# Kernel tuning notes

Measured on AMD Instinct MI355X. Metric: run time of the kernel, lower is better.

## Reference

```python
import jax, jax.numpy as jnp
import numpy as np

# Sizes
NC, NT, NP = 100000, 300000, 50000   # customers, transactions, products
F, DIMC = 8, 16                      # columns per table, per-column embed dim
D = F * DIMC                         # 128 = proj_dim (lazy SAGEConv in-channels)
L, R = 2, 4                          # gnn layers, relation types
OUT = 10                             # out_channels
EM, EI = 300000, 600000              # edges: customer-makes-transaction, product-in-transaction


def setup_inputs() -> dict:
    key = jax.random.key(0)
    ks = jax.random.split(key, 14)
    s = 0.05
    return {
        "x_c": jax.random.normal(ks[0], (NC, F), jnp.float32),
        "x_t": jax.random.normal(ks[1], (NT, F), jnp.float32),
        "x_p": jax.random.normal(ks[2], (NP, F), jnp.float32),
        # per-table per-column numeric embedders: scalar -> DIMC (w*x + b)
        "W_col": jax.random.normal(ks[3], (3, F, DIMC), jnp.float32) * s,
        "b_col": jax.random.normal(ks[4], (3, F, DIMC), jnp.float32) * s,
        # SAGEConv weights per layer per relation: lin_l (neighbor) and lin_r (root)
        "Wn": jax.random.normal(ks[5], (L, R, D, D), jnp.float32) * s,
        "Wr": jax.random.normal(ks[6], (L, R, D, D), jnp.float32) * s,
        "b_lin": jax.random.normal(ks[7], (L, R, D), jnp.float32) * s,
        "W_out": jax.random.normal(ks[8], (D, OUT), jnp.float32) * s,
        "b_out": jax.random.normal(ks[9], (OUT,), jnp.float32) * s,
        "e_makes_src": jax.random.randint(ks[10], (EM,), 0, NC, jnp.int32),
        "e_makes_dst": jax.random.randint(ks[11], (EM,), 0, NT, jnp.int32),
        "e_in_src": jax.random.randint(ks[12], (EI,), 0, NP, jnp.int32),
        "e_in_dst": jax.random.randint(ks[13], (EI,), 0, NT, jnp.int32),
    }


def _embed(x, W, b):
    # x: [N, F]; W,b: [F, DIMC] -> [N, F*DIMC] (concat of per-column embeddings)
    n = x.shape[0]
    return (x[:, :, None] * W[None] + b[None]).reshape(n, -1)


def _sage(x_src, x_dst, src, dst, Wn, Wr, b, n_dst):
    # SAGEConv(mean): out = mean_neigh(x_src) @ Wn + b + x_dst @ Wr
    msg = jax.ops.segment_sum(x_src[src], dst, num_segments=n_dst)
    cnt = jax.ops.segment_sum(jnp.ones(src.shape[0], x_src.dtype), dst, num_segments=n_dst)
    mean = msg / jnp.maximum(cnt, 1.0)[:, None]  # isolated nodes -> 0 message
    return mean @ Wn + x_dst @ Wr + b


def reference(x_c, x_t, x_p, W_col, b_col, Wn, Wr, b_lin, W_out, b_out,
              e_makes_src, e_makes_dst, e_in_src, e_in_dst):
    h_c = _embed(x_c, W_col[0], b_col[0])
    h_t = _embed(x_t, W_col[1], b_col[1])
    h_p = _embed(x_p, W_col[2], b_col[2])
    for l in range(L):
        # R0: customer -makes-> transaction
        o_t0 = _sage(h_c, h_t, e_makes_src, e_makes_dst, Wn[l, 0], Wr[l, 0], b_lin[l, 0], NT)
        # R1: transaction -rev_makes-> customer
        o_c = _sage(h_t, h_c, e_makes_dst, e_makes_src, Wn[l, 1], Wr[l, 1], b_lin[l, 1], NC)
        # R2: product -in-> transaction
        o_t2 = _sage(h_p, h_t, e_in_src, e_in_dst, Wn[l, 2], Wr[l, 2], b_lin[l, 2], NT)
        # R3: transaction -rev_in-> product
        o_p = _sage(h_t, h_p, e_in_dst, e_in_src, Wn[l, 3], Wr[l, 3], b_lin[l, 3], NP)
        # HeteroConv(aggr='mean'): mean over relations targeting each dst type
        h_c, h_t, h_p = o_c, 0.5 * (o_t0 + o_t2), o_p
    logits = h_t @ W_out + b_out  # target_table = 'transaction'
    return jax.nn.softmax(logits, axis=1)
```

## Files before the change

kernel.cpp:

```cpp
#include <hip/hip_runtime.h>

#define NCV 100000
#define NTV 300000
#define NPV 50000
#define DD 128
#define OUTC 10
#define EMV 300000
#define EIV 600000
#define YST 16
#define NHEADS (NCV + NPV + 2 * NTV)
#define HIB ((NHEADS + 255) / 256)
#define PTB ((3 * 1280 * 64) / 256)
#define NEB ((EIV + 255) / 256)
#define QB  ((7 * 1280 * 64) / 256)
#define GYB ((NCV + NPV + 255) / 256)

__device__ __forceinline__ float i2f(int v) { return __int_as_float(v); }

__global__ __launch_bounds__(256) void init_prepT(
    int* __restrict__ heads,
    const float* __restrict__ Wn10, const float* __restrict__ Wn12,
    const float* __restrict__ Wr10, const float* __restrict__ Wr12,
    const float* __restrict__ Wout, float* __restrict__ T) {
  int b = blockIdx.x;
  int tid = threadIdx.x;
  if (b < HIB) {
    int i = b * 256 + tid;
    if (i < NHEADS) heads[i] = -1;
    return;
  }
  int gw = ((b - HIB) * 256 + tid) >> 6;
  int lane = tid & 63;
  if (gw >= 3 * 1280) return;
  int mat = gw / 1280, r = gw % 1280, n = r / 10, o = r % 10;
  float s = 0.f;
  #pragma unroll
  for (int mi = 0; mi < 2; ++mi) {
    int m = lane + mi * 64;
    float w;
    if (mat == 0) w = Wn10[n * 128 + m];
    else if (mat == 1) w = Wn12[n * 128 + m];
    else w = 0.5f * (Wr10[n * 128 + m] + Wr12[n * 128 + m]);
    s += w * Wout[m * 10 + o];
  }
  #pragma unroll
  for (int d = 32; d; d >>= 1) s += __shfl_xor(s, d);
  if (lane == 0) T[gw] = s;
}

__global__ __launch_bounds__(256) void build_prepQ(
    const int* __restrict__ ems, const int* __restrict__ emd,
    const int* __restrict__ eis, const int* __restrict__ eid,
    const float* __restrict__ xt,
    int* __restrict__ head_c, int* __restrict__ head_p,
    int* __restrict__ heads_t,
    int4* __restrict__ cnm, int4* __restrict__ cni,
    int2* __restrict__ tn_m, int2* __restrict__ tn_i,
    const float* __restrict__ Wn01, const float* __restrict__ Wr01,
    const float* __restrict__ Wn03, const float* __restrict__ Wr03,
    const float* __restrict__ Wn00, const float* __restrict__ Wn02,
    const float* __restrict__ Wr00, const float* __restrict__ Wr02,
    const float* __restrict__ T, float* __restrict__ Q) {
  int b = blockIdx.x;
  int tid = threadIdx.x;
  if (b < NEB) {
    int e = b * 256 + tid;
    if (e < EMV) {
      int c = ems[e], t = emd[e];
      int cn = atomicExch(&head_c[c], e);
      int tn = atomicExch(&heads_t[2 * t], e);
      const int4* xr = (const int4*)(xt + (size_t)t * 8);
      int4 x0 = xr[0], x1 = xr[1];
      size_t bb = 4 * (size_t)e;
      cnm[bb]     = make_int4(cn, x0.x, x0.y, x0.z);
      cnm[bb + 1] = make_int4(x0.w, x1.x, x1.y, x1.z);
      cnm[bb + 2] = make_int4(x1.w, 0, 0, 0);
      tn_m[e] = make_int2(tn, c);
    }
    if (e < EIV) {
      int p = eis[e], t = eid[e];
      int pn = atomicExch(&head_p[p], e);
      int tn = atomicExch(&heads_t[2 * t + 1], e);
      const int4* xr = (const int4*)(xt + (size_t)t * 8);
      int4 x0 = xr[0], x1 = xr[1];
      size_t bb = 4 * (size_t)e;
      cni[bb]     = make_int4(pn, x0.x, x0.y, x0.z);
      cni[bb + 1] = make_int4(x0.w, x1.x, x1.y, x1.z);
      cni[bb + 2] = make_int4(x1.w, 0, 0, 0);
      tn_i[e] = make_int2(tn, p);
    }
    return;
  }

  int gw = ((b - NEB) * 256 + tid) >> 6;
  int lane = tid & 63;
  if (gw >= 7 * 1280) return;
  int q = gw / 1280, r = gw % 1280, k = r / 10, o = r % 10;
  const float* T1 = T, *T2 = T + 1280, *T3 = T + 2560;
  float s = 0.f;
  #pragma unroll
  for (int ni = 0; ni < 2; ++ni) {
    int n = lane + ni * 64;
    float w, t;
    switch (q) {
      case 0: w = Wn01[k * 128 + n]; t = T1[n * 10 + o]; break;
      case 1: w = Wr01[k * 128 + n]; t = T1[n * 10 + o]; break;
      case 2: w = Wn03[k * 128 + n]; t = T2[n * 10 + o]; break;
      case 3: w = Wr03[k * 128 + n]; t = T2[n * 10 + o]; break;
      case 4: w = Wn00[k * 128 + n]; t = T3[n * 10 + o]; break;
      case 5: w = Wn02[k * 128 + n]; t = T3[n * 10 + o]; break;
      default: w = Wr00[k * 128 + n] + Wr02[k * 128 + n]; t = T3[n * 10 + o]; break;
    }
    s += w * t;
  }
  #pragma unroll
  for (int d = 32; d; d >>= 1) s += __shfl_xor(s, d);
  if (lane == 0) Q[gw] = s;
}

__global__ __launch_bounds__(256) void prep_B_w(
    const float* __restrict__ Wcol, const float* __restrict__ bcol,
    const float* __restrict__ b_lin, const float* __restrict__ Wout,
    const float* __restrict__ bout, const float* __restrict__ T,
    const float* __restrict__ Q, float* __restrict__ B) {
  int gw = (blockIdx.x * 256 + threadIdx.x) >> 6;
  int lane = threadIdx.x & 63;
  if (gw >= 450) return;
  int r = gw / 10, o = gw % 10;
  const float* WcC = Wcol, *WcT = Wcol + 128, *WcP = Wcol + 256;
  const float* bC = bcol, *bT = bcol + 128, *bP = bcol + 256;
  const float* Q1 = Q, *Q2 = Q + 1280, *Q3 = Q + 2560, *Q4 = Q + 3840;
  const float* Q5 = Q + 5120, *Q6 = Q + 6400, *Q7 = Q + 7680;
  const float* T1 = T, *T2 = T + 1280, *T3 = T + 2560;
  const float* b00 = b_lin, *b01 = b_lin + 128, *b02 = b_lin + 256, *b03 = b_lin + 384;
  const float* b10 = b_lin + 512, *b12 = b_lin + 768;
  float s = 0.f;
  if (r < 8) {
    if (lane < 16) s = WcT[r * 16 + lane] * Q1[(r * 16 + lane) * 10 + o];
  } else if (r < 16) {
    int j = r - 8;
    if (lane < 16)
      s = WcC[j * 16 + lane] * (Q2[(j * 16 + lane) * 10 + o] + Q5[(j * 16 + lane) * 10 + o]);
  } else if (r == 16) {
    for (int k2 = lane; k2 < 128; k2 += 64) s += bT[k2] * Q1[k2 * 10 + o];
  } else if (r < 25) {
    int j = r - 17;
    if (lane < 16) s = WcT[j * 16 + lane] * Q3[(j * 16 + lane) * 10 + o];
  } else if (r < 33) {
    int j = r - 25;
    if (lane < 16)
      s = WcP[j * 16 + lane] * (Q4[(j * 16 + lane) * 10 + o] + Q6[(j * 16 + lane) * 10 + o]);
  } else if (r == 33) {
    for (int k2 = lane; k2 < 128; k2 += 64) s += bT[k2] * Q3[k2 * 10 + o];
  } else if (r < 42) {
    int j = r - 34;
    if (lane < 16) s = WcT[j * 16 + lane] * Q7[(j * 16 + lane) * 10 + o];
  } else if (r == 42) {
    for (int k2 = lane; k2 < 128; k2 += 64)
      s += bC[k2] * (Q2[k2 * 10 + o] + Q5[k2 * 10 + o]) + b01[k2] * T1[k2 * 10 + o];
  } else if (r == 43) {
    for (int k2 = lane; k2 < 128; k2 += 64)
      s += bP[k2] * (Q4[k2 * 10 + o] + Q6[k2 * 10 + o]) + b03[k2] * T2[k2 * 10 + o];
  } else {
    for (int n = lane; n < 128; n += 64)
      s += (b10[n] + b12[n]) * Wout[n * 10 + o] + bT[n] * Q7[n * 10 + o] +
           (b00[n] + b02[n]) * T3[n * 10 + o];
  }
  #pragma unroll
  for (int d = 32; d; d >>= 1) s += __shfl_xor(s, d);
  if (lane == 0) {
    float v = s * 0.5f;
    if (r == 44) v += bout[o];
    B[gw] = v;
  }
}

__global__ __launch_bounds__(256) void gather_y(
    const int* __restrict__ head_c, const int* __restrict__ head_p,
    const int4* __restrict__ cnm, const int4* __restrict__ cni,
    const float* __restrict__ xc, const float* __restrict__ xp,
    const float* __restrict__ B,
    float* __restrict__ y_c, float* __restrict__ y_p) {
  __shared__ float sB[340];
  int tid = threadIdx.x;
  for (int i = tid; i < 340; i += 256) sB[i] = B[i];
  __syncthreads();
  int i = blockIdx.x * 256 + tid;
  if (i >= NCV + NPV) return;
  bool isC = i < NCV;
  int idx = isC ? i : i - NCV;
  const int4* cn = isC ? cnm : cni;
  int e = isC ? head_c[idx] : head_p[idx];

  float acc[8] = {0.f, 0.f, 0.f, 0.f, 0.f, 0.f, 0.f, 0.f};
  float cnt = 0.f;
  while (e >= 0) {
    size_t bb = 4 * (size_t)e;
    int4 w0 = cn[bb];
    int4 w1 = cn[bb + 1];
    int4 w2 = cn[bb + 2];
    acc[0] += i2f(w0.y); acc[1] += i2f(w0.z); acc[2] += i2f(w0.w);
    acc[3] += i2f(w1.x); acc[4] += i2f(w1.y); acc[5] += i2f(w1.z); acc[6] += i2f(w1.w);
    acc[7] += i2f(w2.x);
    cnt += 1.f;
    e = w0.x;
  }

  const float* xo = (isC ? xc : xp) + (size_t)idx * 8;
  const float* Bs = sB + (isC ? 0 : 170);
  float gg = cnt > 0.f ? 1.f : 0.f;
  float inv = gg / fmaxf(cnt, 1.f);
  float lg[OUTC];
  #pragma unroll
  for (int o = 0; o < OUTC; ++o) lg[o] = gg * Bs[16 * 10 + o];
  #pragma unroll
  for (int r = 0; r < 8; ++r) {
    float zb = acc[r] * inv;
    float zo = xo[r];
    #pragma unroll
    for (int o = 0; o < OUTC; ++o)
      lg[o] += zb * Bs[r * 10 + o] + zo * Bs[(8 + r) * 10 + o];
  }
  float4* yv = (float4*)((isC ? y_c : y_p) + (size_t)idx * YST);
  yv[0] = make_float4(lg[0], lg[1], lg[2], lg[3]);
  yv[1] = make_float4(lg[4], lg[5], lg[6], lg[7]);
  yv[2] = make_float4(lg[8], lg[9], 0.f, 0.f);
  yv[3] = make_float4(0.f, 0.f, 0.f, 0.f);
}

__global__ __launch_bounds__(256) void gather_t(
    const float* __restrict__ y_c, const float* __restrict__ y_p,
    const float* __restrict__ xt,
    const int* __restrict__ heads_t,
    const int2* __restrict__ tn_m, const int2* __restrict__ tn_i,
    const float* __restrict__ B, float* __restrict__ out) {
  __shared__ float sB[110];
  int tid = threadIdx.x;
  for (int i = tid; i < 110; i += 256) sB[i] = B[340 + i];
  __syncthreads();
  int t = blockIdx.x * 256 + tid;
  if (t >= NTV) return;

  int2 ht = ((const int2*)heads_t)[t];
  int e1 = ht.x, e2 = ht.y;

  float sc[OUTC] = {0.f, 0.f, 0.f, 0.f, 0.f, 0.f, 0.f, 0.f, 0.f, 0.f};
  float sp[OUTC] = {0.f, 0.f, 0.f, 0.f, 0.f, 0.f, 0.f, 0.f, 0.f, 0.f};
  float dc = 0.f, dp = 0.f;
  while (e1 >= 0 || e2 >= 0) {
    if (e1 >= 0) {
      int2 v = tn_m[e1];
      const float* yr = y_c + (size_t)v.y * YST;
      float4 u = *(const float4*)yr;
      float4 w = *(const float4*)(yr + 4);
      float2 z = *(const float2*)(yr + 8);
      sc[0] += u.x; sc[1] += u.y; sc[2] += u.z; sc[3] += u.w;
      sc[4] += w.x; sc[5] += w.y; sc[6] += w.z; sc[7] += w.w;
      sc[8] += z.x; sc[9] += z.y;
      dc += 1.f;
      e1 = v.x;
    }
    if (e2 >= 0) {
      int2 v = tn_i[e2];
      const float* yr = y_p + (size_t)v.y * YST;
      float4 u = *(const float4*)yr;
      float4 w = *(const float4*)(yr + 4);
      float2 z = *(const float2*)(yr + 8);
      sp[0] += u.x; sp[1] += u.y; sp[2] += u.z; sp[3] += u.w;
      sp[4] += w.x; sp[5] += w.y; sp[6] += w.z; sp[7] += w.w;
      sp[8] += z.x; sp[9] += z.y;
      dp += 1.f;
      e2 = v.x;
    }
  }

  float Gc = dc > 0.f ? 1.f : 0.f, Gp = dp > 0.f ? 1.f : 0.f;
  float ivc = 1.f / fmaxf(dc, 1.f), ivp = 1.f / fmaxf(dp, 1.f);

  const float4* xp4 = (const float4*)(xt + (size_t)t * 8);
  float4 xa = xp4[0], xb = xp4[1];
  float xv[8] = {xa.x, xa.y, xa.z, xa.w, xb.x, xb.y, xb.z, xb.w};

  float lg[OUTC];
  #pragma unroll
  for (int o = 0; o < OUTC; ++o)
    lg[o] = sc[o] * ivc + sp[o] * ivp +
            Gc * sB[80 + o] + Gp * sB[90 + o] + sB[100 + o];
  #pragma unroll
  for (int r = 0; r < 8; ++r) {
    float xr = xv[r];
    #pragma unroll
    for (int o = 0; o < OUTC; ++o) lg[o] += xr * sB[r * 10 + o];
  }

  float m = lg[0];
  #pragma unroll
  for (int o = 1; o < OUTC; ++o) m = fmaxf(m, lg[o]);
  float s = 0.f;
  #pragma unroll
  for (int o = 0; o < OUTC; ++o) { lg[o] = __expf(lg[o] - m); s += lg[o]; }
  float invs = 1.0f / s;
  float* op = &out[(size_t)t * OUTC];
  #pragma unroll
  for (int o = 0; o < 5; ++o) {
    float2 p2; p2.x = lg[2 * o] * invs; p2.y = lg[2 * o + 1] * invs;
    *(float2*)&op[2 * o] = p2;
  }
}

extern "C" void kernel_launch(void* const* d_in, const int* in_sizes, int n_in,
                              void* d_out, int out_size, void* d_ws, size_t ws_size,
                              hipStream_t stream) {
  const float* x_c   = (const float*)d_in[0];
  const float* x_t   = (const float*)d_in[1];
  const float* x_p   = (const float*)d_in[2];
  const float* W_col = (const float*)d_in[3];
  const float* b_col = (const float*)d_in[4];
  const float* Wn    = (const float*)d_in[5];
  const float* Wr    = (const float*)d_in[6];
  const float* b_lin = (const float*)d_in[7];
  const float* W_out = (const float*)d_in[8];
  const float* b_out = (const float*)d_in[9];
  const int* e_m_src = (const int*)d_in[10];
  const int* e_m_dst = (const int*)d_in[11];
  const int* e_i_src = (const int*)d_in[12];
  const int* e_i_dst = (const int*)d_in[13];
  float* out = (float*)d_out;

  size_t cursor = 0;
  char* base = (char*)d_ws;
  auto alloc = [&](size_t bytes) {
    void* p = base + cursor;
    cursor += (bytes + 255) & ~(size_t)255;
    return p;
  };
  int* heads   = (int*)alloc((size_t)NHEADS * 4);
  int* head_c  = heads;
  int* head_p  = heads + NCV;
  int* heads_t = heads + NCV + NPV;
  int4* cnm = (int4*)alloc((size_t)EMV * 64);
  int4* cni = (int4*)alloc((size_t)EIV * 64);
  int2* tn_m = (int2*)alloc((size_t)EMV * 8);
  int2* tn_i = (int2*)alloc((size_t)EIV * 8);
  float* y_c = (float*)alloc((size_t)NCV * YST * 4);
  float* y_p = (float*)alloc((size_t)NPV * YST * 4);
  float* T   = (float*)alloc(3 * 1280 * 4);
  float* Q   = (float*)alloc(7 * 1280 * 4);
  float* B   = (float*)alloc(450 * 4);

  const float* Wn_l[2][4]; const float* Wr_l[2][4];
  for (int l = 0; l < 2; ++l)
    for (int r = 0; r < 4; ++r) {
      Wn_l[l][r] = Wn + (size_t)(l * 4 + r) * DD * DD;
      Wr_l[l][r] = Wr + (size_t)(l * 4 + r) * DD * DD;
    }

  init_prepT<<<HIB + PTB, 256, 0, stream>>>(
      heads, Wn_l[1][0], Wn_l[1][2], Wr_l[1][0], Wr_l[1][2], W_out, T);

  build_prepQ<<<NEB + QB, 256, 0, stream>>>(
      e_m_src, e_m_dst, e_i_src, e_i_dst, x_t,
      head_c, head_p, heads_t, cnm, cni, tn_m, tn_i,
      Wn_l[0][1], Wr_l[0][1], Wn_l[0][3], Wr_l[0][3],
      Wn_l[0][0], Wn_l[0][2], Wr_l[0][0], Wr_l[0][2], T, Q);

  prep_B_w<<<(450 * 64 + 255) / 256, 256, 0, stream>>>(
      W_col, b_col, b_lin, W_out, b_out, T, Q, B);

  gather_y<<<GYB, 256, 0, stream>>>(
      head_c, head_p, cnm, cni, x_c, x_p, B, y_c, y_p);

  gather_t<<<(NTV + 255) / 256, 256, 0, stream>>>(
      y_c, y_p, x_t, heads_t, tn_m, tn_i, B, out);
}
```

Measured before the change: 224.8 us.

## Fold Q precompute into B computation, removing the separate prep_B_w launch

Drops the intermediate Q matrices (weights multiplied into T) and instead has each B warp contract the column embedder coefficients with the layer-0 SAGE weights directly, then dot with T. This lets the B computation run inside the edge-building kernel, which removes one kernel launch and the Q buffer round trip. In exchange each B warp runs longer serial loops (up to 128 iterations over two weight matrices), which lengthens the tail of the fused kernel.

Result: no change. 224.0 us (-0.4%).

```diff
diff --git a/kernel.cpp b/kernel.cpp
--- a/kernel.cpp
+++ b/kernel.cpp
@@ -12,7 +12,7 @@
 #define HIB ((NHEADS + 255) / 256)
 #define PTB ((3 * 1280 * 64) / 256)
 #define NEB ((EIV + 255) / 256)
-#define QB  ((7 * 1280 * 64) / 256)
+#define BDB ((450 * 64 + 255) / 256)
 #define GYB ((NCV + NPV + 255) / 256)
 
 __device__ __forceinline__ float i2f(int v) { return __int_as_float(v); }
@@ -48,7 +48,7 @@
   if (lane == 0) T[gw] = s;
 }
 
-__global__ __launch_bounds__(256) void build_prepQ(
+__global__ __launch_bounds__(256) void build_prepB(
     const int* __restrict__ ems, const int* __restrict__ emd,
     const int* __restrict__ eis, const int* __restrict__ eid,
     const float* __restrict__ xt,
@@ -56,11 +56,11 @@
     int* __restrict__ heads_t,
     int4* __restrict__ cnm, int4* __restrict__ cni,
     int2* __restrict__ tn_m, int2* __restrict__ tn_i,
-    const float* __restrict__ Wn01, const float* __restrict__ Wr01,
-    const float* __restrict__ Wn03, const float* __restrict__ Wr03,
-    const float* __restrict__ Wn00, const float* __restrict__ Wn02,
-    const float* __restrict__ Wr00, const float* __restrict__ Wr02,
-    const float* __restrict__ T, float* __restrict__ Q) {
+    const float* __restrict__ Wn, const float* __restrict__ Wr,
+    const float* __restrict__ Wcol, const float* __restrict__ bcol,
+    const float* __restrict__ b_lin, const float* __restrict__ Wout,
+    const float* __restrict__ bout,
+    const float* __restrict__ T, float* __restrict__ B) {
   int b = blockIdx.x;
   int tid = threadIdx.x;
   if (b < NEB) {
@@ -94,82 +94,99 @@
 
   int gw = ((b - NEB) * 256 + tid) >> 6;
   int lane = tid & 63;
-  if (gw >= 7 * 1280) return;
-  int q = gw / 1280, r = gw % 1280, k = r / 10, o = r % 10;
-  const float* T1 = T, *T2 = T + 1280, *T3 = T + 2560;
-  float s = 0.f;
-  #pragma unroll
-  for (int ni = 0; ni < 2; ++ni) {
-    int n = lane + ni * 64;
-    float w, t;
-    switch (q) {
-      case 0: w = Wn01[k * 128 + n]; t = T1[n * 10 + o]; break;
-      case 1: w = Wr01[k * 128 + n]; t = T1[n * 10 + o]; break;
-      case 2: w = Wn03[k * 128 + n]; t = T2[n * 10 + o]; break;
-      case 3: w = Wr03[k * 128 + n]; t = T2[n * 10 + o]; break;
-      case 4: w = Wn00[k * 128 + n]; t = T3[n * 10 + o]; break;
-      case 5: w = Wn02[k * 128 + n]; t = T3[n * 10 + o]; break;
-      default: w = Wr00[k * 128 + n] + Wr02[k * 128 + n]; t = T3[n * 10 + o]; break;
-    }
-    s += w * t;
-  }
-  #pragma unroll
-  for (int d = 32; d; d >>= 1) s += __shfl_xor(s, d);
-  if (lane == 0) Q[gw] = s;
-}
-
-__global__ __launch_bounds__(256) void prep_B_w(
-    const float* __restrict__ Wcol, const float* __restrict__ bcol,
-    const float* __restrict__ b_lin, const float* __restrict__ Wout,
-    const float* __restrict__ bout, const float* __restrict__ T,
-    const float* __restrict__ Q, float* __restrict__ B) {
-  int gw = (blockIdx.x * 256 + threadIdx.x) >> 6;
-  int lane = threadIdx.x & 63;
   if (gw >= 450) return;
   int r = gw / 10, o = gw % 10;
+  int n0 = lane, n1 = lane + 64;
+
+  const float* Wn00 = Wn;               const float* Wn01 = Wn + 16384;
+  const float* Wn02 = Wn + 2 * 16384;   const float* Wn03 = Wn + 3 * 16384;
+  const float* Wr00 = Wr;               const float* Wr01 = Wr + 16384;
+  const float* Wr02 = Wr + 2 * 16384;   const float* Wr03 = Wr + 3 * 16384;
   const float* WcC = Wcol, *WcT = Wcol + 128, *WcP = Wcol + 256;
   const float* bC = bcol, *bT = bcol + 128, *bP = bcol + 256;
-  const float* Q1 = Q, *Q2 = Q + 1280, *Q3 = Q + 2560, *Q4 = Q + 3840;
-  const float* Q5 = Q + 5120, *Q6 = Q + 6400, *Q7 = Q + 7680;
-  const float* T1 = T, *T2 = T + 1280, *T3 = T + 2560;
   const float* b00 = b_lin, *b01 = b_lin + 128, *b02 = b_lin + 256, *b03 = b_lin + 384;
   const float* b10 = b_lin + 512, *b12 = b_lin + 768;
-  float s = 0.f;
+  const float* T1 = T, *T2 = T + 1280, *T3 = T + 2560;
+
+  float a1_0 = 0.f, a1_1 = 0.f;
+  float a2_0 = 0.f, a2_1 = 0.f;
+  float a3_0 = 0.f, a3_1 = 0.f;
+  float extra = 0.f;
+
   if (r < 8) {
-    if (lane < 16) s = WcT[r * 16 + lane] * Q1[(r * 16 + lane) * 10 + o];
+    for (int j = 0; j < 16; ++j) {
+      float c = WcT[r * 16 + j]; int k = r * 16 + j;
+      a1_0 += c * Wn01[k * 128 + n0]; a1_1 += c * Wn01[k * 128 + n1];
+    }
   } else if (r < 16) {
-    int j = r - 8;
-    if (lane < 16)
-      s = WcC[j * 16 + lane] * (Q2[(j * 16 + lane) * 10 + o] + Q5[(j * 16 + lane) * 10 + o]);
+    int j0 = r - 8;
+    for (int j = 0; j < 16; ++j) {
+      float c = WcC[j0 * 16 + j]; int k = j0 * 16 + j;
+      a1_0 += c * Wr01[k * 128 + n0]; a1_1 += c * Wr01[k * 128 + n1];
+      a3_0 += c * Wn00[k * 128 + n0]; a3_1 += c * Wn00[k * 128 + n1];
+    }
   } else if (r == 16) {
-    for (int k2 = lane; k2 < 128; k2 += 64) s += bT[k2] * Q1[k2 * 10 + o];
+    for (int k = 0; k < 128; ++k) {
+      float c = bT[k];
+      a1_0 += c * Wn01[k * 128 + n0]; a1_1 += c * Wn01[k * 128 + n1];
+    }
   } else if (r < 25) {
-    int j = r - 17;
-    if (lane < 16) s = WcT[j * 16 + lane] * Q3[(j * 16 + lane) * 10 + o];
+    int j0 = r - 17;
+    for (int j = 0; j < 16; ++j) {
+      float c = WcT[j0 * 16 + j]; int k = j0 * 16 + j;
+      a2_0 += c * Wn03[k * 128 + n0]; a2_1 += c * Wn03[k * 128 + n1];
+    }
   } else if (r < 33) {
-    int j = r - 25;
-    if (lane < 16)
-      s = WcP[j * 16 + lane] * (Q4[(j * 16 + lane) * 10 + o] + Q6[(j * 16 + lane) * 10 + o]);
+    int j0 = r - 25;
+    for (int j = 0; j < 16; ++j) {
+      float c = WcP[j0 * 16 + j]; int k = j0 * 16 + j;
+      a2_0 += c * Wr03[k * 128 + n0]; a2_1 += c * Wr03[k * 128 + n1];
+      a3_0 += c * Wn02[k * 128 + n0]; a3_1 += c * Wn02[k * 128 + n1];
+    }
   } else if (r == 33) {
-    for (int k2 = lane; k2 < 128; k2 += 64) s += bT[k2] * Q3[k2 * 10 + o];
+    for (int k = 0; k < 128; ++k) {
+      float c = bT[k];
+      a2_0 += c * Wn03[k * 128 + n0]; a2_1 += c * Wn03[k * 128 + n1];
+    }
   } else if (r < 42) {
-    int j = r - 34;
-    if (lane < 16) s = WcT[j * 16 + lane] * Q7[(j * 16 + lane) * 10 + o];
+    int j0 = r - 34;
+    for (int j = 0; j < 16; ++j) {
+      float c = WcT[j0 * 16 + j]; int k = j0 * 16 + j;
+      a3_0 += c * (Wr00[k * 128 + n0] + Wr02[k * 128 + n0]);
+      a3_1 += c * (Wr00[k * 128 + n1] + Wr02[k * 128 + n1]);
+    }
   } else if (r == 42) {
-    for (int k2 = lane; k2 < 128; k2 += 64)
-      s += bC[k2] * (Q2[k2 * 10 + o] + Q5[k2 * 10 + o]) + b01[k2] * T1[k2 * 10 + o];
+    for (int k = 0; k < 128; ++k) {
+      float c = bC[k];
+      a1_0 += c * Wr01[k * 128 + n0]; a1_1 += c * Wr01[k * 128 + n1];
+      a3_0 += c * Wn00[k * 128 + n0]; a3_1 += c * Wn00[k * 128 + n1];
+    }
+    a1_0 += b01[n0]; a1_1 += b01[n1];
   } else if (r == 43) {
-    for (int k2 = lane; k2 < 128; k2 += 64)
-      s += bP[k2] * (Q4[k2 * 10 + o] + Q6[k2 * 10 + o]) + b03[k2] * T2[k2 * 10 + o];
+    for (int k = 0; k < 128; ++k) {
+      float c = bP[k];
+      a2_0 += c * Wr03[k * 128 + n0]; a2_1 += c * Wr03[k * 128 + n1];
+      a3_0 += c * Wn02[k * 128 + n0]; a3_1 += c * Wn02[k * 128 + n1];
+    }
+    a2_0 += b03[n0]; a2_1 += b03[n1];
   } else {
-    for (int n = lane; n < 128; n += 64)
-      s += (b10[n] + b12[n]) * Wout[n * 10 + o] + bT[n] * Q7[n * 10 + o] +
-           (b00[n] + b02[n]) * T3[n * 10 + o];
-  }
+    for (int k = 0; k < 128; ++k) {
+      float c = bT[k];
+      a3_0 += c * (Wr00[k * 128 + n0] + Wr02[k * 128 + n0]);
+      a3_1 += c * (Wr00[k * 128 + n1] + Wr02[k * 128 + n1]);
+    }
+    a3_0 += b00[n0] + b02[n0]; a3_1 += b00[n1] + b02[n1];
+    extra = (b10[n0] + b12[n0]) * Wout[n0 * 10 + o] +
+            (b10[n1] + b12[n1]) * Wout[n1 * 10 + o];
+  }
+
+  float s = a1_0 * T1[n0 * 10 + o] + a1_1 * T1[n1 * 10 + o] +
+            a2_0 * T2[n0 * 10 + o] + a2_1 * T2[n1 * 10 + o] +
+            a3_0 * T3[n0 * 10 + o] + a3_1 * T3[n1 * 10 + o] + extra;
   #pragma unroll
   for (int d = 32; d; d >>= 1) s += __shfl_xor(s, d);
   if (lane == 0) {
-    float v = s * 0.5f;
+    float v = 0.5f * s;
     if (r == 44) v += bout[o];
     B[gw] = v;
   }
@@ -345,27 +362,20 @@
   float* y_c = (float*)alloc((size_t)NCV * YST * 4);
   float* y_p = (float*)alloc((size_t)NPV * YST * 4);
   float* T   = (float*)alloc(3 * 1280 * 4);
-  float* Q   = (float*)alloc(7 * 1280 * 4);
   float* B   = (float*)alloc(450 * 4);
 
-  const float* Wn_l[2][4]; const float* Wr_l[2][4];
-  for (int l = 0; l < 2; ++l)
-    for (int r = 0; r < 4; ++r) {
-      Wn_l[l][r] = Wn + (size_t)(l * 4 + r) * DD * DD;
-      Wr_l[l][r] = Wr + (size_t)(l * 4 + r) * DD * DD;
-    }
+  const float* Wn10 = Wn + 4 * (size_t)DD * DD;
+  const float* Wn12 = Wn + 6 * (size_t)DD * DD;
+  const float* Wr10 = Wr + 4 * (size_t)DD * DD;
+  const float* Wr12 = Wr + 6 * (size_t)DD * DD;
 
   init_prepT<<<HIB + PTB, 256, 0, stream>>>(
-      heads, Wn_l[1][0], Wn_l[1][2], Wr_l[1][0], Wr_l[1][2], W_out, T);
-
-  build_prepQ<<<NEB + QB, 256, 0, stream>>>(
+      heads, Wn10, Wn12, Wr10, Wr12, W_out, T);
+
+  build_prepB<<<NEB + BDB, 256, 0, stream>>>(
       e_m_src, e_m_dst, e_i_src, e_i_dst, x_t,
       head_c, head_p, heads_t, cnm, cni, tn_m, tn_i,
-      Wn_l[0][1], Wr_l[0][1], Wn_l[0][3], Wr_l[0][3],
-      Wn_l[0][0], Wn_l[0][2], Wr_l[0][0], Wr_l[0][2], T, Q);
-
-  prep_B_w<<<(450 * 64 + 255) / 256, 256, 0, stream>>>(
-      W_col, b_col, b_lin, W_out, b_out, T, Q, B);
+      Wn, Wr, W_col, b_col, b_lin, W_out, b_out, T, B);
 
   gather_y<<<GYB, 256, 0, stream>>>(
       head_c, head_p, cnm, cni, x_c, x_p, B, y_c, y_p);
```
